# Performance work log

Hardware: AMD Instinct MI355X
Metric: run time of the kernel (lower is better)

Reference implementation:

```python
import jax, jax.numpy as jnp
import numpy as np

B, L, D, N = 4, 8192, 128, 32


def setup_inputs() -> dict:
    key = jax.random.key(0)
    ks = jax.random.split(key, 12)
    s = 0.05  # small init scale for stability of exp/cumsum
    return {
        "x": jax.random.normal(ks[0], (B, L, D), jnp.float32),
        "h_t_minus_1": jax.random.normal(ks[1], (B, L, D), jnp.float32),
        "A_log": jax.random.normal(ks[2], (D, N), jnp.float32),
        "D_param": jnp.ones((D,), jnp.float32),
        "W_x": jax.random.normal(ks[3], (D, 2 * N + D), jnp.float32) * s,
        "W_dt": jax.random.normal(ks[4], (D, D), jnp.float32) * s,
        "b_dt": jnp.zeros((D,), jnp.float32),
        "conv_w": jax.random.normal(ks[5], (3, D, D), jnp.float32) * s,  # (width, in, out)
        "conv_b": jnp.zeros((D,), jnp.float32),
        "W_f": jax.random.normal(ks[6], (D, D), jnp.float32) * s,
        "b_f": jnp.zeros((D,), jnp.float32),
    }


def reference(x, h_t_minus_1, A_log, D_param, W_x, W_dt, b_dt, conv_w, conv_b, W_f, b_f):
    d, n = A_log.shape
    A = -jnp.exp(A_log)  # (d, n)
    x_dbl = x @ W_x  # (b, l, d + 2n)
    delta, Bm, Cm = jnp.split(x_dbl, [d, d + n], axis=-1)
    delta = jax.nn.softplus(delta @ W_dt + b_dt)  # (b, l, d)

    # selective scan
    dA = jnp.einsum('bld,dn->bldn', delta, A)
    dB_u = jnp.einsum('bld,bld,bln->bldn', delta, h_t_minus_1, Bm)
    dA_cumsum = jnp.exp(jnp.cumsum(dA, axis=1) - dA)  # exclusive cumsum
    h_t = jnp.einsum('bldn,bln->bld', dB_u * dA_cumsum, Cm)
    h_t = h_t + h_t * D_param

    ssm_output = jax.nn.relu(h_t @ W_f + b_f)
    # causal Conv1D, kernel=3: left-pad by 2
    conv = jax.lax.conv_general_dilated(
        ssm_output, conv_w, window_strides=(1,), padding=[(2, 0)],
        dimension_numbers=('NWC', 'WIO', 'NWC')) + conv_b
    causal_output = jax.nn.relu(conv)
    fused_output = ssm_output * causal_output
    return (fused_output, h_t)
```

## Files before the change

kernel.cpp:

```cpp
#include <hip/hip_runtime.h>
#include <math.h>

typedef unsigned short u16;
typedef __attribute__((ext_vector_type(8))) short short8v;
typedef __attribute__((ext_vector_type(4))) float f32x4;

constexpr int B_  = 4;
constexpr int L_  = 8192;
constexpr int D_  = 128;
constexpr int N_  = 32;
constexpr int BL  = B_ * L_;
constexpr int CH  = 16;
constexpr int NC  = L_ / CH;
constexpr int SCH = 32;
constexpr int SNC = L_ / SCH;

__device__ inline unsigned bfr(float x) {
    unsigned u = __float_as_uint(x);
    return (u + 0x7fffu + ((u >> 16) & 1u)) >> 16;
}
__device__ inline unsigned pkbf(float a, float b) { return bfr(a) | (bfr(b) << 16); }
__device__ inline float b2f(u16 h) { return __uint_as_float(((unsigned)h) << 16); }

__global__ __launch_bounds__(512) void prep_weff(
    const float* __restrict__ Wx, const float* __restrict__ Wdt,
    u16* __restrict__ Wt0)
{
    __shared__ float wd[128 * 128];
    const int tid = threadIdx.x;
    #pragma unroll
    for (int j = 0; j < 8; ++j) {
        const int g = tid + j * 512;
        *reinterpret_cast<float4*>(&wd[g * 4]) =
            *reinterpret_cast<const float4*>(&Wdt[(size_t)g * 4]);
    }
    __syncthreads();
    const int k = blockIdx.x * 4 + (tid >> 7);
    const int d = tid & 127;
    float s = 0.f;
    #pragma unroll 8
    for (int j = 0; j < 128; ++j)
        s = fmaf(Wx[(size_t)k * 192 + j], wd[j * 128 + d], s);
    Wt0[d * 128 + k] = (u16)bfr(s);
}

__global__ __launch_bounds__(256) void prep_rest(
    const float* __restrict__ Wx, const float* __restrict__ Wf,
    const float* __restrict__ Wconv, const float* __restrict__ A_log,
    u16* __restrict__ Wt0, u16* __restrict__ Wt2, u16* __restrict__ Wtc,
    float* __restrict__ negAT, float* __restrict__ amax)
{
    const int which = blockIdx.y;
    const int t = blockIdx.x * 256 + threadIdx.x;
    constexpr float L2E = 1.4426950408889634f;
    if (which == 0) {
        if (t >= 64 * 128) return;
        const int n = t >> 7, k = t & 127;
        Wt0[(128 + n) * 128 + k] = (u16)bfr(Wx[(size_t)k * 192 + 128 + n]);
    } else if (which == 1) {
        if (t >= 128 * 128) return;
        const int n = t >> 7, k = t & 127;
        Wt2[n * 128 + k] = (u16)bfr(Wf[(size_t)k * 128 + n]);
    } else if (which <= 4) {
        if (t >= 128 * 128) return;
        const int w = which - 2;
        const int n = t >> 7, k = t & 127;
        Wtc[((size_t)w * 128 + n) * 128 + k] = (u16)bfr(Wconv[((size_t)w * 128 + k) * 128 + n]);
    } else if (which == 5) {
        if (t >= 128 * 32) return;
        const int d = t >> 5, n = t & 31;
        negAT[n * 128 + d] = -expf(A_log[d * 32 + n]) * L2E;
    } else {
        if (t >= 128) return;
        float m = -1e30f;
        for (int n = 0; n < 32; ++n)
            m = fmaxf(m, -expf(A_log[t * 32 + n]) * L2E);
        amax[t] = m;
    }
}

__global__ __launch_bounds__(256) void gemm1(
    const float* __restrict__ x, const u16* __restrict__ Wt0,
    const float* __restrict__ b_dt,
    float* __restrict__ delta, float* __restrict__ Sloc,
    float* __restrict__ bc, float* __restrict__ part)
{
    __shared__ __align__(16) u16 Blds[192 * 128];

    const int tid = threadIdx.x;
    const int r0 = blockIdx.x * 64;

    #pragma unroll
    for (int j = 0; j < 12; ++j) {
        const int g = tid + j * 256;
        const int n = g >> 4, k8 = (g & 15) * 8;
        const uint4 p = *reinterpret_cast<const uint4*>(&Wt0[(size_t)n * 128 + k8]);
        *reinterpret_cast<uint4*>(&Blds[n * 128 + (k8 ^ ((n & 7) << 3))]) = p;
    }

    const int w = tid >> 6, lane = tid & 63;
    const int lr = lane & 15, kg = lane >> 4;
    const int arow = r0 + w * 16 + lr;

    float4 av[4][2];
    #pragma unroll
    for (int ks = 0; ks < 4; ++ks) {
        const float* src = &x[(size_t)arow * 128 + ks * 32 + kg * 8];
        av[ks][0] = *reinterpret_cast<const float4*>(src);
        av[ks][1] = *reinterpret_cast<const float4*>(src + 4);
    }
    __syncthreads();

    f32x4 acc[12] = {};
    #pragma unroll
    for (int ks = 0; ks < 4; ++ks) {
        uint4 ap;
        ap.x = pkbf(av[ks][0].x, av[ks][0].y);
        ap.y = pkbf(av[ks][0].z, av[ks][0].w);
        ap.z = pkbf(av[ks][1].x, av[ks][1].y);
        ap.w = pkbf(av[ks][1].z, av[ks][1].w);
        const short8v af = *reinterpret_cast<const short8v*>(&ap);
        const int kb = ks * 32 + kg * 8;
        #pragma unroll
        for (int nf = 0; nf < 12; ++nf) {
            const int n = nf * 16 + lr;
            const short8v bf = *reinterpret_cast<const short8v*>(
                &Blds[n * 128 + (kb ^ ((n & 7) << 3))]);
            acc[nf] = __builtin_amdgcn_mfma_f32_16x16x32_bf16(af, bf, acc[nf], 0, 0, 0);
        }
    }

    const int orow = r0 + w * 16;
    const size_t chunkb = (size_t)(orow / CH) * 128;
    #pragma unroll
    for (int nf = 0; nf < 8; ++nf) {
        const int col = nf * 16 + lr;
        const float bb = b_dt[col];
        float v[4];
        #pragma unroll
        for (int q = 0; q < 4; ++q) {
            const float t = acc[nf][q] + bb;
            v[q] = fmaxf(t, 0.f) + log1pf(expf(-fabsf(t)));
        }
        const float e1 = v[0], e2 = e1 + v[1], e3 = e2 + v[2];
        const float g4 = e3 + v[3];
        const float g0 = __shfl(g4, lr, 64);
        const float g1 = __shfl(g4, lr + 16, 64);
        const float g2 = __shfl(g4, lr + 32, 64);
        const float g3 = __shfl(g4, lr + 48, 64);
        float base = 0.f;
        if (kg > 0) base += g0;
        if (kg > 1) base += g1;
        if (kg > 2) base += g2;
        const size_t rb = (size_t)(orow + kg * 4) * 128 + col;
        delta[rb + 0 * 128] = v[0];
        delta[rb + 1 * 128] = v[1];
        delta[rb + 2 * 128] = v[2];
        delta[rb + 3 * 128] = v[3];
        Sloc[rb + 0 * 128] = base;
        Sloc[rb + 1 * 128] = base + e1;
        Sloc[rb + 2 * 128] = base + e2;
        Sloc[rb + 3 * 128] = base + e3;
        if (kg == 0) part[chunkb + col] = g0 + g1 + g2 + g3;
    }
    #pragma unroll
    for (int h = 0; h < 2; ++h)
        #pragma unroll
        for (int q = 0; q < 4; ++q)
            bc[(size_t)(orow + kg * 4 + q) * 32 + h * 16 + lr] =
                acc[8 + h][q] * acc[10 + h][q];
}

__global__ __launch_bounds__(512) void scan_prefix(float* __restrict__ part)
{
    const int b = blockIdx.x, d = blockIdx.y;
    const int c = threadIdx.x, w = c >> 6, lane = c & 63;
    const size_t idx = ((size_t)b * NC + c) * 128 + d;
    const float v = part[idx];
    float s = v;
    #pragma unroll
    for (int off = 1; off < 64; off <<= 1) {
        const float t = __shfl_up(s, off, 64);
        if (lane >= off) s += t;
    }
    __shared__ float wsum[8];
    if (lane == 63) wsum[w] = s;
    __syncthreads();
    float add = 0.f;
    #pragma unroll
    for (int i = 0; i < 8; ++i)
        if (i < w) add += wsum[i];
    part[idx] = s + add - v;
}

__global__ __launch_bounds__(512) void scan_main(
    const float* __restrict__ delta, const float* __restrict__ Sloc,
    const float* __restrict__ hprev, const float* __restrict__ bc,
    const float* __restrict__ negAT, const float* __restrict__ amax,
    const float* __restrict__ Dp, const float* __restrict__ part,
    const u16* __restrict__ Wt2, const float* __restrict__ b_f,
    float* __restrict__ h_out, u16* __restrict__ ssm)
{
    __shared__ float at_s[32 * 128];
    __shared__ float bc_s[SCH * 32];
    __shared__ __align__(16) u16 h_s[SCH * 128];

    const int cb = blockIdx.x, b = blockIdx.y;
    const int tid = threadIdx.x;
    const size_t rowbase = (size_t)b * L_ + (size_t)cb * SCH;

    #pragma unroll
    for (int j = 0; j < 2; ++j) {
        const int g = tid + j * 512;
        reinterpret_cast<float4*>(at_s)[g] =
            reinterpret_cast<const float4*>(negAT)[g];
    }
    if (tid < 256)
        reinterpret_cast<float4*>(bc_s)[tid] =
            reinterpret_cast<const float4*>(&bc[rowbase * 32])[tid];

    const int d = tid & 127, r0 = tid >> 7;
    const float dp1 = 1.f + Dp[d];
    const float am = amax[d];
    const size_t pbase = ((size_t)b * NC + (size_t)cb * 2) * 128 + d;
    const float part0 = part[pbase];
    const float part1 = part[pbase + 128];
    __syncthreads();

    for (int r = 0; r < 8; ++r) {
        const int i = r * 4 + r0;
        const size_t rb = (rowbase + i) * 128 + d;
        const float S = ((i < 16) ? part0 : part1) + Sloc[rb];
        float h = 0.f;
        const int need = (S * am >= -80.f);
        if (__any(need)) {
            const float dv = delta[rb];
            const float hv = hprev[rb];
            float p0 = 0.f, p1 = 0.f, p2 = 0.f, p3 = 0.f;
            #pragma unroll
            for (int n4 = 0; n4 < 8; ++n4) {
                const float4 b4 = *reinterpret_cast<const float4*>(&bc_s[i * 32 + n4 * 4]);
                p0 = fmaf(b4.x, exp2f(S * at_s[(n4 * 4 + 0) * 128 + d]), p0);
                p1 = fmaf(b4.y, exp2f(S * at_s[(n4 * 4 + 1) * 128 + d]), p1);
                p2 = fmaf(b4.z, exp2f(S * at_s[(n4 * 4 + 2) * 128 + d]), p2);
                p3 = fmaf(b4.w, exp2f(S * at_s[(n4 * 4 + 3) * 128 + d]), p3);
            }
            h = dv * hv * ((p0 + p1) + (p2 + p3)) * dp1;
        }
        h_out[rb] = h;
        h_s[i * 128 + (((d >> 3) ^ (i & 7)) << 3) + (d & 7)] = (u16)bfr(h);
    }
    __syncthreads();

    const int wid = tid >> 6, lane = tid & 63;
    const int lr = lane & 15, kg = lane >> 4;
    const int col = wid * 16 + lr;
    f32x4 acc[2] = {};
    #pragma unroll
    for (int ks = 0; ks < 4; ++ks) {
        const int k8 = ks * 32 + kg * 8;
        const short8v bfg = *reinterpret_cast<const short8v*>(&Wt2[(size_t)col * 128 + k8]);
        #pragma unroll
        for (int m = 0; m < 2; ++m) {
            const int row = m * 16 + lr;
            const short8v afg = *reinterpret_cast<const short8v*>(
                &h_s[row * 128 + (k8 ^ ((row & 7) << 3))]);
            acc[m] = __builtin_amdgcn_mfma_f32_16x16x32_bf16(afg, bfg, acc[m], 0, 0, 0);
        }
    }
    const float bb = b_f[col];
    #pragma unroll
    for (int m = 0; m < 2; ++m)
        #pragma unroll
        for (int q = 0; q < 4; ++q) {
            const int row = m * 16 + kg * 4 + q;
            const float v = fmaxf(acc[m][q] + bb, 0.f);
            ssm[(rowbase + row) * 128 + col] = (u16)bfr(v);
        }
}

__global__ __launch_bounds__(512) void conv_fuse(
    const u16* __restrict__ ssm, const u16* __restrict__ Wtc,
    const float* __restrict__ cbias, float* __restrict__ fused)
{
    __shared__ __align__(16) u16 Alds[66 * 128];

    const int tid = threadIdx.x;
    const int bb = blockIdx.y;
    const int r0 = blockIdx.x * 64;
    const u16* sb = ssm + (size_t)bb * L_ * 128;

    #pragma unroll
    for (int j = 0; j < 3; ++j) {
        const int g = tid + j * 512;
        if (g < 66 * 16) {
            const int i = g >> 4, k8 = (g & 15) * 8;
            const int gr = r0 - 2 + i;
            uint4 p = make_uint4(0, 0, 0, 0);
            if (gr >= 0)
                p = *reinterpret_cast<const uint4*>(&sb[(size_t)gr * 128 + k8]);
            *reinterpret_cast<uint4*>(&Alds[i * 128 + (k8 ^ ((i & 7) << 3))]) = p;
        }
    }
    __syncthreads();

    const int wid = tid >> 6, lane = tid & 63;
    const int wm = wid >> 2, wn = wid & 3;
    const int lr = lane & 15, kg = lane >> 4;

    f32x4 acc[2][2] = {};
    #pragma unroll
    for (int ks = 0; ks < 4; ++ks) {
        const int k8 = ks * 32 + kg * 8;
        short8v af[2][3];
        #pragma unroll
        for (int m = 0; m < 2; ++m)
            #pragma unroll
            for (int w = 0; w < 3; ++w) {
                const int ri = wm * 32 + m * 16 + lr + w;
                af[m][w] = *reinterpret_cast<const short8v*>(
                    &Alds[ri * 128 + (k8 ^ ((ri & 7) << 3))]);
            }
        #pragma unroll
        for (int nf = 0; nf < 2; ++nf) {
            const int col = wn * 32 + nf * 16 + lr;
            #pragma unroll
            for (int w = 0; w < 3; ++w) {
                const short8v bfg = *reinterpret_cast<const short8v*>(
                    &Wtc[((size_t)w * 128 + col) * 128 + k8]);
                acc[0][nf] = __builtin_amdgcn_mfma_f32_16x16x32_bf16(af[0][w], bfg, acc[0][nf], 0, 0, 0);
                acc[1][nf] = __builtin_amdgcn_mfma_f32_16x16x32_bf16(af[1][w], bfg, acc[1][nf], 0, 0, 0);
            }
        }
    }

    #pragma unroll
    for (int nf = 0; nf < 2; ++nf) {
        const int col = wn * 32 + nf * 16 + lr;
        const float bb2 = cbias[col];
        #pragma unroll
        for (int m = 0; m < 2; ++m)
            #pragma unroll
            for (int q = 0; q < 4; ++q) {
                const int row = wm * 32 + m * 16 + kg * 4 + q;
                const int ri = row + 2;
                const u16 sh = Alds[ri * 128 + ((((col >> 3) ^ (ri & 7)) << 3)) + (col & 7)];
                const float cv = fmaxf(acc[m][nf][q] + bb2, 0.f);
                fused[((size_t)bb * L_ + r0 + row) * 128 + col] = b2f(sh) * cv;
            }
    }
}

extern "C" void kernel_launch(void* const* d_in, const int* in_sizes, int n_in,
                              void* d_out, int out_size, void* d_ws, size_t ws_size,
                              hipStream_t stream)
{
    const float* x      = (const float*)d_in[0];
    const float* hprev  = (const float*)d_in[1];
    const float* A_log  = (const float*)d_in[2];
    const float* Dp     = (const float*)d_in[3];
    const float* W_x    = (const float*)d_in[4];
    const float* W_dt   = (const float*)d_in[5];
    const float* b_dt   = (const float*)d_in[6];
    const float* conv_w = (const float*)d_in[7];
    const float* conv_b = (const float*)d_in[8];
    const float* W_f    = (const float*)d_in[9];
    const float* b_f    = (const float*)d_in[10];

    float* out   = (float*)d_out;
    float* h_out = out + (size_t)BL * D_;

    char* ws = (char*)d_ws;
    float* delta = (float*)ws;                  ws += (size_t)BL * 128 * 4;
    float* sloc  = (float*)ws;                  ws += (size_t)BL * 128 * 4;
    float* bcb   = (float*)ws;                  ws += (size_t)BL * 32 * 4;
    float* part  = (float*)ws;                  ws += (size_t)B_ * NC * 128 * 4;
    float* negAT = (float*)ws;                  ws += (size_t)N_ * 128 * 4;
    float* amaxb = (float*)ws;                  ws += (size_t)128 * 4;
    u16*   Wt0   = (u16*)ws;                    ws += (size_t)192 * 128 * 2;
    u16*   Wt2   = (u16*)ws;                    ws += (size_t)128 * 128 * 2;
    u16*   Wtc   = (u16*)ws;                    ws += (size_t)3 * 128 * 128 * 2;
    u16*   ssm   = (u16*)ws;

    prep_weff<<<dim3(32), dim3(512), 0, stream>>>(W_x, W_dt, Wt0);
    prep_rest<<<dim3(64, 7), dim3(256), 0, stream>>>(
        W_x, W_f, conv_w, A_log, Wt0, Wt2, Wtc, negAT, amaxb);
    gemm1<<<dim3(BL / 64), dim3(256), 0, stream>>>(
        x, Wt0, b_dt, delta, sloc, bcb, part);
    scan_prefix<<<dim3(B_, D_), dim3(512), 0, stream>>>(part);
    scan_main<<<dim3(SNC, B_), dim3(512), 0, stream>>>(
        delta, sloc, hprev, bcb, negAT, amaxb, Dp, part, Wt2, b_f, h_out, ssm);
    conv_fuse<<<dim3(L_ / 64, B_), dim3(512), 0, stream>>>(
        ssm, Wtc, conv_b, out);
}
```

Measured before the change: 171.5 us.

## Drop Sloc buffer; recompute in-chunk prefix from LDS-staged delta in scan

The gemm1 kernel no longer writes a full per-element local prefix-sum array (Sloc). scan_main instead stages its chunk's delta tile in shared memory and recomputes the running sum per column from the chunk prefix. This removes one BL×128 float write and read from global memory. The partial-sum layout is transposed so scan_prefix reads are contiguous, and gemm1 now uses 128-row, 512-thread blocks. The cost is extra LDS use and a short serial prefix loop in scan_main.

```diff
diff --git a/kernel.cpp b/kernel.cpp
--- a/kernel.cpp
+++ b/kernel.cpp
@@ -79,20 +79,20 @@
     }
 }
 
-__global__ __launch_bounds__(256) void gemm1(
+__global__ __launch_bounds__(512) void gemm1(
     const float* __restrict__ x, const u16* __restrict__ Wt0,
     const float* __restrict__ b_dt,
-    float* __restrict__ delta, float* __restrict__ Sloc,
-    float* __restrict__ bc, float* __restrict__ part)
+    float* __restrict__ delta, float* __restrict__ bc,
+    float* __restrict__ part)
 {
     __shared__ __align__(16) u16 Blds[192 * 128];
 
     const int tid = threadIdx.x;
-    const int r0 = blockIdx.x * 64;
-
-    #pragma unroll
-    for (int j = 0; j < 12; ++j) {
-        const int g = tid + j * 256;
+    const int R0 = blockIdx.x * 128;
+
+    #pragma unroll
+    for (int j = 0; j < 6; ++j) {
+        const int g = tid + j * 512;
         const int n = g >> 4, k8 = (g & 15) * 8;
         const uint4 p = *reinterpret_cast<const uint4*>(&Wt0[(size_t)n * 128 + k8]);
         *reinterpret_cast<uint4*>(&Blds[n * 128 + (k8 ^ ((n & 7) << 3))]) = p;
@@ -100,7 +100,7 @@
 
     const int w = tid >> 6, lane = tid & 63;
     const int lr = lane & 15, kg = lane >> 4;
-    const int arow = r0 + w * 16 + lr;
+    const int arow = R0 + w * 16 + lr;
 
     float4 av[4][2];
     #pragma unroll
@@ -130,53 +130,46 @@
         }
     }
 
-    const int orow = r0 + w * 16;
-    const size_t chunkb = (size_t)(orow / CH) * 128;
+    const int orow = R0 + w * 16;
+    const int bb = orow >> 13;
+    const int chk = (orow & (L_ - 1)) >> 4;
     #pragma unroll
     for (int nf = 0; nf < 8; ++nf) {
         const int col = nf * 16 + lr;
-        const float bb = b_dt[col];
+        const float bbv = b_dt[col];
         float v[4];
         #pragma unroll
         for (int q = 0; q < 4; ++q) {
-            const float t = acc[nf][q] + bb;
+            const float t = acc[nf][q] + bbv;
             v[q] = fmaxf(t, 0.f) + log1pf(expf(-fabsf(t)));
         }
-        const float e1 = v[0], e2 = e1 + v[1], e3 = e2 + v[2];
-        const float g4 = e3 + v[3];
+        const float g4 = v[0] + v[1] + v[2] + v[3];
         const float g0 = __shfl(g4, lr, 64);
         const float g1 = __shfl(g4, lr + 16, 64);
         const float g2 = __shfl(g4, lr + 32, 64);
         const float g3 = __shfl(g4, lr + 48, 64);
-        float base = 0.f;
-        if (kg > 0) base += g0;
-        if (kg > 1) base += g1;
-        if (kg > 2) base += g2;
         const size_t rb = (size_t)(orow + kg * 4) * 128 + col;
         delta[rb + 0 * 128] = v[0];
         delta[rb + 1 * 128] = v[1];
         delta[rb + 2 * 128] = v[2];
         delta[rb + 3 * 128] = v[3];
-        Sloc[rb + 0 * 128] = base;
-        Sloc[rb + 1 * 128] = base + e1;
-        Sloc[rb + 2 * 128] = base + e2;
-        Sloc[rb + 3 * 128] = base + e3;
-        if (kg == 0) part[chunkb + col] = g0 + g1 + g2 + g3;
-    }
-    #pragma unroll
-    for (int h = 0; h < 2; ++h)
+        if (kg == 0)
+            part[((size_t)bb * 128 + col) * NC + chk] = g0 + g1 + g2 + g3;
+    }
+    #pragma unroll
+    for (int h2 = 0; h2 < 2; ++h2)
         #pragma unroll
         for (int q = 0; q < 4; ++q)
-            bc[(size_t)(orow + kg * 4 + q) * 32 + h * 16 + lr] =
-                acc[8 + h][q] * acc[10 + h][q];
+            bc[(size_t)(orow + kg * 4 + q) * 32 + h2 * 16 + lr] =
+                acc[8 + h2][q] * acc[10 + h2][q];
 }
 
 __global__ __launch_bounds__(512) void scan_prefix(float* __restrict__ part)
 {
     const int b = blockIdx.x, d = blockIdx.y;
     const int c = threadIdx.x, w = c >> 6, lane = c & 63;
-    const size_t idx = ((size_t)b * NC + c) * 128 + d;
-    const float v = part[idx];
+    const size_t base = ((size_t)b * 128 + d) * NC;
+    const float v = part[base + c];
     float s = v;
     #pragma unroll
     for (int off = 1; off < 64; off <<= 1) {
@@ -190,17 +183,18 @@
     #pragma unroll
     for (int i = 0; i < 8; ++i)
         if (i < w) add += wsum[i];
-    part[idx] = s + add - v;
+    part[base + c] = s + add - v;
 }
 
 __global__ __launch_bounds__(512) void scan_main(
-    const float* __restrict__ delta, const float* __restrict__ Sloc,
-    const float* __restrict__ hprev, const float* __restrict__ bc,
-    const float* __restrict__ negAT, const float* __restrict__ amax,
-    const float* __restrict__ Dp, const float* __restrict__ part,
+    const float* __restrict__ delta, const float* __restrict__ hprev,
+    const float* __restrict__ bc, const float* __restrict__ negAT,
+    const float* __restrict__ amax, const float* __restrict__ Dp,
+    const float* __restrict__ part,
     const u16* __restrict__ Wt2, const float* __restrict__ b_f,
     float* __restrict__ h_out, u16* __restrict__ ssm)
 {
+    __shared__ float delta_s[SCH * 128];
     __shared__ float at_s[32 * 128];
     __shared__ float bc_s[SCH * 32];
     __shared__ __align__(16) u16 h_s[SCH * 128];
@@ -209,6 +203,12 @@
     const int tid = threadIdx.x;
     const size_t rowbase = (size_t)b * L_ + (size_t)cb * SCH;
 
+    #pragma unroll
+    for (int j = 0; j < 2; ++j) {
+        const int g = tid + j * 512;
+        reinterpret_cast<float4*>(delta_s)[g] =
+            reinterpret_cast<const float4*>(&delta[rowbase * 128])[g];
+    }
     #pragma unroll
     for (int j = 0; j < 2; ++j) {
         const int g = tid + j * 512;
@@ -222,24 +222,40 @@
     const int d = tid & 127, r0 = tid >> 7;
     const float dp1 = 1.f + Dp[d];
     const float am = amax[d];
-    const size_t pbase = ((size_t)b * NC + (size_t)cb * 2) * 128 + d;
-    const float part0 = part[pbase];
-    const float part1 = part[pbase + 128];
-    __syncthreads();
-
+    const size_t pb = ((size_t)b * 128 + d) * NC + (size_t)cb * 2;
+    const float part0 = part[pb];
+    const float part1 = part[pb + 1];
+    __syncthreads();
+
+    float sv[8];
+    {
+        float s = part0;
+        #pragma unroll
+        for (int i = 0; i < 16; ++i) {
+            if ((i & 3) == r0) sv[i >> 2] = s;
+            s += delta_s[i * 128 + d];
+        }
+        s = part1;
+        #pragma unroll
+        for (int i = 16; i < 32; ++i) {
+            if ((i & 3) == r0) sv[i >> 2] = s;
+            s += delta_s[i * 128 + d];
+        }
+    }
+
+    #pragma unroll 1
     for (int r = 0; r < 8; ++r) {
-        const int i = r * 4 + r0;
-        const size_t rb = (rowbase + i) * 128 + d;
-        const float S = ((i < 16) ? part0 : part1) + Sloc[rb];
+        const int row = r * 4 + r0;
+        const size_t rb = (rowbase + row) * 128 + d;
+        const float S = sv[r];
         float h = 0.f;
-        const int need = (S * am >= -80.f);
-        if (__any(need)) {
-            const float dv = delta[rb];
+        if (__any(S * am >= -80.f)) {
+            const float dv = delta_s[row * 128 + d];
             const float hv = hprev[rb];
             float p0 = 0.f, p1 = 0.f, p2 = 0.f, p3 = 0.f;
             #pragma unroll
             for (int n4 = 0; n4 < 8; ++n4) {
-                const float4 b4 = *reinterpret_cast<const float4*>(&bc_s[i * 32 + n4 * 4]);
+                const float4 b4 = *reinterpret_cast<const float4*>(&bc_s[row * 32 + n4 * 4]);
                 p0 = fmaf(b4.x, exp2f(S * at_s[(n4 * 4 + 0) * 128 + d]), p0);
                 p1 = fmaf(b4.y, exp2f(S * at_s[(n4 * 4 + 1) * 128 + d]), p1);
                 p2 = fmaf(b4.z, exp2f(S * at_s[(n4 * 4 + 2) * 128 + d]), p2);
@@ -248,7 +264,7 @@
             h = dv * hv * ((p0 + p1) + (p2 + p3)) * dp1;
         }
         h_out[rb] = h;
-        h_s[i * 128 + (((d >> 3) ^ (i & 7)) << 3) + (d & 7)] = (u16)bfr(h);
+        h_s[row * 128 + (d ^ ((row & 7) << 3))] = (u16)bfr(h);
     }
     __syncthreads();
 
@@ -372,9 +388,8 @@
 
     char* ws = (char*)d_ws;
     float* delta = (float*)ws;                  ws += (size_t)BL * 128 * 4;
-    float* sloc  = (float*)ws;                  ws += (size_t)BL * 128 * 4;
     float* bcb   = (float*)ws;                  ws += (size_t)BL * 32 * 4;
-    float* part  = (float*)ws;                  ws += (size_t)B_ * NC * 128 * 4;
+    float* part  = (float*)ws;                  ws += (size_t)B_ * 128 * NC * 4;
     float* negAT = (float*)ws;                  ws += (size_t)N_ * 128 * 4;
     float* amaxb = (float*)ws;                  ws += (size_t)128 * 4;
     u16*   Wt0   = (u16*)ws;                    ws += (size_t)192 * 128 * 2;
@@ -385,11 +400,11 @@
     prep_weff<<<dim3(32), dim3(512), 0, stream>>>(W_x, W_dt, Wt0);
     prep_rest<<<dim3(64, 7), dim3(256), 0, stream>>>(
         W_x, W_f, conv_w, A_log, Wt0, Wt2, Wtc, negAT, amaxb);
-    gemm1<<<dim3(BL / 64), dim3(256), 0, stream>>>(
-        x, Wt0, b_dt, delta, sloc, bcb, part);
+    gemm1<<<dim3(BL / 128), dim3(512), 0, stream>>>(
+        x, Wt0, b_dt, delta, bcb, part);
     scan_prefix<<<dim3(B_, D_), dim3(512), 0, stream>>>(part);
     scan_main<<<dim3(SNC, B_), dim3(512), 0, stream>>>(
-        delta, sloc, hprev, bcb, negAT, amaxb, Dp, part, Wt2, b_f, h_out, ssm);
+        delta, hprev, bcb, negAT, amaxb, Dp, part, Wt2, b_f, h_out, ssm);
     conv_fuse<<<dim3(L_ / 64, B_), dim3(512), 0, stream>>>(
         ssm, Wtc, conv_b, out);
 }
```

After: 168.9 us. Within noise of the previous version (-1.5%).
